# Optimization experiments

Hardware: AMD Instinct MI355X
Metric: run time of the kernel (lower is better)

## Reference

```python
import jax, jax.numpy as jnp
import numpy as np
from math import sqrt

DIM = 256

def setup_inputs() -> dict:
    key = jax.random.key(0)
    k1, k2, k3, k4 = jax.random.split(key, 4)
    B, T, D, H, R = 2, 4096, DIM, 8, 32
    # xavier-uniform-ish scaled params
    def xavier(k, shape, fan_in, fan_out):
        a = sqrt(6.0 / (fan_in + fan_out))
        return jax.random.uniform(k, shape, jnp.float32, -a, a)
    x = jax.random.normal(k1, (B, T, D), jnp.float32)
    Q = xavier(k2, (H, R, D), D, R)
    K = xavier(k3, (H, R, D), D, R)
    VO = xavier(k4, (H, D, D), D, D)
    return {"x": x, "Q": Q, "K": K, "VO": VO}

def reference(x, Q, K, VO):
    # x: [b,t,d]; Q,K: [h,r,d]; VO: [h,d,e]
    d = x.shape[-1]
    q = jnp.einsum('btd,hrd->bhtr', x, Q)          # low-rank query proj
    k = jnp.einsum('bud,hrd->bhur', x, K)          # low-rank key proj
    scores = jnp.einsum('bhtr,bhur->bhtu', q, k) / sqrt(d)
    attn = jax.nn.softmax(scores, axis=-1)         # softmax over u (keys)
    ctx = jnp.einsum('bhtu,bud->bhtd', attn, x)    # values are raw x
    out = jnp.einsum('bhtd,hde->bte', ctx, VO)     # fused value-output proj, summed over heads
    return out
```

## Files before the change

### kernel.cpp

```cpp
#include <hip/hip_runtime.h>
#include <hip/hip_bf16.h>
#include <cstdint>
#include <cstddef>

typedef __attribute__((ext_vector_type(8))) __bf16 bf16x8;
typedef __attribute__((ext_vector_type(4))) float f32x4;
typedef __attribute__((ext_vector_type(16))) float f32x16;

#define MFMA16(a, b, c) __builtin_amdgcn_mfma_f32_16x16x32_bf16((a), (b), (c), 0, 0, 0)
#define MFMA32(a, b, c) __builtin_amdgcn_mfma_f32_32x32x16_bf16((a), (b), (c), 0, 0, 0)
#define MFMA8(a, b, c)  __builtin_amdgcn_mfma_f32_32x32x16_fp8_fp8((a), (b), (c), 0, 0, 0)

__device__ __forceinline__ f32x16 zf16() {
    f32x16 z;
    #pragma unroll
    for (int r = 0; r < 16; ++r) z[r] = 0.f;
    return z;
}

__device__ __forceinline__ void swap32(unsigned& a, unsigned& b) {
    asm("v_permlane32_swap_b32 %0, %1" : "+v"(a), "+v"(b));
}

__global__ __launch_bounds__(256) void prep(const float* __restrict__ x,
                                            const float* __restrict__ Qw,
                                            const float* __restrict__ Kw,
                                            const float* __restrict__ VO,
                                            unsigned char* __restrict__ x8T,
                                            __bf16* __restrict__ xrow,
                                            __bf16* __restrict__ wb,
                                            __bf16* __restrict__ vot) {
    __shared__ float tile[64][65];
    const int bid = blockIdx.x;
    if (bid < 512) {
        const int b = bid >> 8;
        const int rem = bid & 255;
        const int tt = rem >> 2, dd = rem & 3;
        const int t0 = tt * 64, d0 = dd * 64;
        #pragma unroll
        for (int j = 0; j < 16; ++j) {
            int idx = j * 256 + threadIdx.x;
            int t = idx >> 6, d = idx & 63;
            float v = x[((size_t)(b * 4096 + t0 + t)) * 256 + d0 + d];
            tile[t][d] = v;
            xrow[((size_t)(b * 4096 + t0 + t)) * 256 + d0 + d] = (__bf16)v;
        }
        __syncthreads();
        #pragma unroll
        for (int j = 0; j < 8; ++j) {
            int idx = j * 256 + threadIdx.x;
            int d = idx >> 5, tp = idx & 31;
            float v0 = tile[tp * 2][d];
            float v1 = tile[tp * 2 + 1][d];
            int wpk = __builtin_amdgcn_cvt_pk_fp8_f32(v0, v1, 0, false);
            *(unsigned short*)(x8T + (size_t)(b * 256 + d0 + d) * 4096 + t0 + tp * 2) =
                (unsigned short)wpk;
        }
    } else if (bid < 640) {
        const int k = bid - 512;
        const int h = k >> 4;
        const int rem = k & 15;
        const int dt = rem >> 2, et = rem & 3;
        const int d0 = dt * 64, e0 = et * 64;
        #pragma unroll
        for (int j = 0; j < 16; ++j) {
            int idx = j * 256 + threadIdx.x;
            int d = idx >> 6, e = idx & 63;
            tile[d][e] = VO[((size_t)(h * 256 + d0 + d)) * 256 + e0 + e];
        }
        __syncthreads();
        #pragma unroll
        for (int j = 0; j < 16; ++j) {
            int idx = j * 256 + threadIdx.x;
            int e = idx >> 6, d = idx & 63;
            vot[((size_t)(e0 + e)) * 2048 + h * 256 + d0 + d] = (__bf16)tile[d][e];
        }
    } else {
        const float cl = 1.4426950408889634f / 16.0f;
        #pragma unroll
        for (int e = 0; e < 2; ++e) {
            int i = (bid - 640) * 512 + e * 256 + threadIdx.x;
            float v = (i < 65536) ? Qw[i] * cl : Kw[i - 65536];
            wb[i] = (__bf16)v;
        }
    }
}

__global__ __launch_bounds__(256) void proj_kernel(const __bf16* __restrict__ xrow,
                                                   const __bf16* __restrict__ wb,
                                                   __bf16* __restrict__ qo,
                                                   __bf16* __restrict__ ko) {
    const int w = threadIdx.x >> 6;
    const int l = threadIdx.x & 63;
    const int g = l >> 4, c = l & 15;
    const int tg = blockIdx.x * 64 + w * 16;

    bf16x8 af[8];
    #pragma unroll
    for (int kk = 0; kk < 8; ++kk)
        af[kk] = *(const bf16x8*)(xrow + (size_t)(tg + c) * 256 + kk * 32 + g * 8);

    const int b = tg >> 12, t = tg & 4095;
    #pragma unroll
    for (int hs = 0; hs < 16; ++hs) {
        const int h = hs >> 1, s = hs & 1;
        const __bf16* W = wb + (size_t)(s * 8 + h) * 8192;
        f32x4 acc0 = {0.f, 0.f, 0.f, 0.f}, acc1 = {0.f, 0.f, 0.f, 0.f};
        #pragma unroll
        for (int kk = 0; kk < 8; ++kk) {
            bf16x8 b0 = *(const bf16x8*)(W + (size_t)c * 256 + kk * 32 + g * 8);
            bf16x8 b1 = *(const bf16x8*)(W + (size_t)(16 + c) * 256 + kk * 32 + g * 8);
            acc0 = MFMA16(af[kk], b0, acc0);
            acc1 = MFMA16(af[kk], b1, acc1);
        }
        __bf16* outp = s ? ko : qo;
        const size_t obase = (size_t)(b * 8 + h) * 4096 + t;
        #pragma unroll
        for (int i = 0; i < 4; ++i) {
            outp[(obase + 4 * g + i) * 32 + c]      = (__bf16)acc0[i];
            outp[(obase + 4 * g + i) * 32 + 16 + c] = (__bf16)acc1[i];
        }
    }
}


#define MK8FRAG(dst, V, base)                                                  \
    {                                                                          \
        unsigned d0 = 0, d1 = 0;                                               \
        d0 = __builtin_amdgcn_cvt_pk_fp8_f32(V[(base) + 0], V[(base) + 1], d0, false); \
        d0 = __builtin_amdgcn_cvt_pk_fp8_f32(V[(base) + 2], V[(base) + 3], d0, true);  \
        d1 = __builtin_amdgcn_cvt_pk_fp8_f32(V[(base) + 4], V[(base) + 5], d1, false); \
        d1 = __builtin_amdgcn_cvt_pk_fp8_f32(V[(base) + 6], V[(base) + 7], d1, true);  \
        swap32(d0, d1);                                                        \
        union { unsigned u[2]; long l; } z;                                    \
        z.u[0] = d0; z.u[1] = d1;                                              \
        dst = z.l;                                                             \
    }

__global__ __launch_bounds__(512, 2) void attn_kernel(const __bf16* __restrict__ qg,
                                                      const __bf16* __restrict__ kg,
                                                      const unsigned char* __restrict__ x8g,
                                                      __bf16* __restrict__ ctx) {
    __shared__ __align__(16) unsigned char lds[2 * 18432 + 1024];
    unsigned char* xbuf0 = lds;
    unsigned char* xbuf1 = lds + 18432;
    float* scale_base = (float*)(lds + 36864);

    const int bid = blockIdx.x;
    const int bh = bid >> 4;
    const int tt = bid & 15;
    const int b = bh >> 3, h = bh & 7;
    const int t0 = tt * 256;
    const int tid = threadIdx.x;
    const int w = tid >> 6;
    const int l = tid & 63;
    const int l31 = l & 31, hi = l >> 5;

    float* scale_w = scale_base + w * 32;

    const unsigned char* x8b = x8g + (size_t)b * 256 * 4096;
    const __bf16* kg_bh = kg + (size_t)bh * 4096 * 32;

    const int srow = tid >> 1;
    const int soff = (tid & 1) * 32;

    const size_t qoff = ((size_t)bh * 4096 + t0 + w * 32 + l31) * 32;
    const bf16x8 qf0 = *(const bf16x8*)(qg + qoff + hi * 8);
    const bf16x8 qf1 = *(const bf16x8*)(qg + qoff + 16 + hi * 8);

    f32x16 acc[8];
    #pragma unroll
    for (int n = 0; n < 8; ++n)
        #pragma unroll
        for (int r = 0; r < 16; ++r) acc[n][r] = 0.f;

    float lsum = 0.f;

    bf16x8 kA[2][2];
    #pragma unroll
    for (int s = 0; s < 2; ++s)
        #pragma unroll
        for (int st = 0; st < 2; ++st)
            kA[s][st] = *(const bf16x8*)(kg_bh + (size_t)(s * 32 + l31) * 32 + st * 16 + hi * 8);

    {
        const unsigned char* sp = x8b + (size_t)srow * 4096 + soff;
        uint4 la = *(const uint4*)sp;
        uint4 lb = *(const uint4*)(sp + 16);
        unsigned char* dp = xbuf0 + srow * 72 + soff;
        union { uint4 v; unsigned long long q[2]; } ua, ub;
        ua.v = la; ub.v = lb;
        ((unsigned long long*)dp)[0] = ua.q[0];
        ((unsigned long long*)dp)[1] = ua.q[1];
        ((unsigned long long*)(dp + 16))[0] = ub.q[0];
        ((unsigned long long*)(dp + 16))[1] = ub.q[1];
    }
    __syncthreads();

    for (int ut = 0; ut < 64; ++ut) {
        unsigned char* xcur = (ut & 1) ? xbuf1 : xbuf0;
        unsigned char* xnxt = (ut & 1) ? xbuf0 : xbuf1;

        const int u_next = ((ut + 1) & 63) * 64;
        const unsigned char* sp = x8b + (size_t)srow * 4096 + u_next + soff;
        const uint4 la = *(const uint4*)sp;
        const uint4 lb = *(const uint4*)(sp + 16);

        f32x16 s0 = MFMA32(kA[0][0], qf0, zf16());
        s0 = MFMA32(kA[0][1], qf1, s0);
        f32x16 s1 = MFMA32(kA[1][0], qf0, zf16());
        s1 = MFMA32(kA[1][1], qf1, s1);

        if (ut < 63) {
            const __bf16* kp = kg_bh + (size_t)(ut + 1) * 64 * 32;
            #pragma unroll
            for (int s = 0; s < 2; ++s)
                #pragma unroll
                for (int st = 0; st < 2; ++st)
                    kA[s][st] = *(const bf16x8*)(kp + (size_t)(s * 32 + l31) * 32 + st * 16 + hi * 8);
        }

        float rs = 0.f;
        #pragma unroll
        for (int r = 0; r < 16; ++r) {
            float p = __builtin_amdgcn_exp2f(s0[r]);
            s0[r] = p; rs += p;
        }
        #pragma unroll
        for (int r = 0; r < 16; ++r) {
            float p = __builtin_amdgcn_exp2f(s1[r]);
            s1[r] = p; rs += p;
        }
        lsum += rs;

        long pf0, pf1, pf2, pf3;
        MK8FRAG(pf0, s0, 0);
        MK8FRAG(pf1, s0, 8);
        MK8FRAG(pf2, s1, 0);
        MK8FRAG(pf3, s1, 8);

        __builtin_amdgcn_s_setprio(1);
        #pragma unroll
        for (int kk = 0; kk < 4; ++kk) {
            const long pa = (kk == 0) ? pf0 : (kk == 1) ? pf1 : (kk == 2) ? pf2 : pf3;
            #pragma unroll
            for (int n = 0; n < 8; ++n) {
                const long xb = *(const long*)(xcur + (n * 32 + l31) * 72 + kk * 16 + hi * 8);
                acc[n] = MFMA8(pa, xb, acc[n]);
            }
        }
        __builtin_amdgcn_s_setprio(0);

        {
            unsigned char* dp = xnxt + srow * 72 + soff;
            union { uint4 v; unsigned long long q[2]; } ua, ub;
            ua.v = la; ub.v = lb;
            ((unsigned long long*)dp)[0] = ua.q[0];
            ((unsigned long long*)dp)[1] = ua.q[1];
            ((unsigned long long*)(dp + 16))[0] = ub.q[0];
            ((unsigned long long*)(dp + 16))[1] = ub.q[1];
        }
        __syncthreads();
    }

    lsum += __shfl_xor(lsum, 32);
    const float linv = 1.0f / lsum;
    if (!hi) scale_w[l31] = linv;
    f32x4 iv[4];
    #pragma unroll
    for (int q4 = 0; q4 < 4; ++q4)
        iv[q4] = *(const f32x4*)&scale_w[q4 * 8 + hi * 4];
    #pragma unroll
    for (int n = 0; n < 8; ++n) {
        #pragma unroll
        for (int r = 0; r < 16; ++r) {
            int t = t0 + w * 32 + (r & 3) + 8 * (r >> 2) + 4 * hi;
            int d = n * 32 + l31;
            ctx[((size_t)(b * 4096 + t) * 8 + h) * 256 + d] =
                (__bf16)(acc[n][r] * iv[r >> 2][r & 3]);
        }
    }
}

__global__ __launch_bounds__(256) void gemm_out(const __bf16* __restrict__ ctx,
                                                const __bf16* __restrict__ vot,
                                                float* __restrict__ out) {
    const int bid = blockIdx.x;
    const int mt2 = bid >> 1;
    const int eh = bid & 1;
    const int w = threadIdx.x >> 6;
    const int l = threadIdx.x & 63;
    const int l31 = l & 31, hi = l >> 5;
    const size_t a0row = (size_t)(mt2 * 64 + l31) * 2048;
    const size_t a1row = (size_t)(mt2 * 64 + 32 + l31) * 2048;
    const size_t brow  = (size_t)(eh * 128 + w * 32 + l31) * 2048;
    f32x16 acc0 = zf16(), acc1 = zf16();
    #pragma unroll 4
    for (int kk = 0; kk < 128; ++kk) {
        bf16x8 bfr = *(const bf16x8*)(vot + brow + kk * 16 + hi * 8);
        bf16x8 a0  = *(const bf16x8*)(ctx + a0row + kk * 16 + hi * 8);
        bf16x8 a1  = *(const bf16x8*)(ctx + a1row + kk * 16 + hi * 8);
        acc0 = MFMA32(a0, bfr, acc0);
        acc1 = MFMA32(a1, bfr, acc1);
    }
    const int e = eh * 128 + w * 32 + l31;
    #pragma unroll
    for (int r = 0; r < 16; ++r) {
        int crow = (r & 3) + 8 * (r >> 2) + 4 * hi;
        out[(size_t)(mt2 * 64 + crow) * 256 + e]      = acc0[r];
        out[(size_t)(mt2 * 64 + 32 + crow) * 256 + e] = acc1[r];
    }
}

extern "C" void kernel_launch(void* const* d_in, const int* in_sizes, int n_in,
                              void* d_out, int out_size, void* d_ws, size_t ws_size,
                              hipStream_t stream) {
    const float* x  = (const float*)d_in[0];
    const float* Qw = (const float*)d_in[1];
    const float* Kw = (const float*)d_in[2];
    const float* VO = (const float*)d_in[3];
    float* out = (float*)d_out;

    char* ws = (char*)d_ws;
    unsigned char* x8 = (unsigned char*)(ws);
    __bf16* xrow = (__bf16*)(ws + ((size_t)4 << 20));
    __bf16* qb   = (__bf16*)(ws + ((size_t)8 << 20));
    __bf16* kb   = (__bf16*)(ws + ((size_t)12 << 20));
    __bf16* wb   = (__bf16*)(ws + ((size_t)16 << 20));
    __bf16* vot  = (__bf16*)(ws + ((size_t)17 << 20));
    __bf16* ctx  = (__bf16*)(ws + ((size_t)18 << 20));

    prep<<<896, 256, 0, stream>>>(x, Qw, Kw, VO, x8, xrow, wb, vot);
    proj_kernel<<<128, 256, 0, stream>>>(xrow, wb, qb, kb);
    attn_kernel<<<256, 512, 0, stream>>>(qb, kb, x8, ctx);
    gemm_out<<<256, 256, 0, stream>>>(ctx, vot, out);
}
```

Before: 213.5 us.

## Split attention blocks into 128-query tiles with 256 threads each

Halves the attention block from 512 to 256 threads (4 waves covering 128 queries) and doubles the grid to 512 blocks. Each thread now stages a full 64-byte row of the fp8 x tile into LDS instead of half a row. This gives more blocks across the CUs and better load balance, but each block reloads the whole K and x streams, doubling global and L2 traffic for x8 and K.

```diff
diff --git a/kernel.cpp b/kernel.cpp
--- a/kernel.cpp
+++ b/kernel.cpp
@@ -137,20 +137,20 @@
         dst = z.l;                                                             \
     }
 
-__global__ __launch_bounds__(512, 2) void attn_kernel(const __bf16* __restrict__ qg,
+__global__ __launch_bounds__(256, 2) void attn_kernel(const __bf16* __restrict__ qg,
                                                       const __bf16* __restrict__ kg,
                                                       const unsigned char* __restrict__ x8g,
                                                       __bf16* __restrict__ ctx) {
-    __shared__ __align__(16) unsigned char lds[2 * 18432 + 1024];
+    __shared__ __align__(16) unsigned char lds[2 * 18432 + 512];
     unsigned char* xbuf0 = lds;
     unsigned char* xbuf1 = lds + 18432;
     float* scale_base = (float*)(lds + 36864);
 
     const int bid = blockIdx.x;
-    const int bh = bid >> 4;
-    const int tt = bid & 15;
+    const int bh = bid >> 5;
+    const int tt = bid & 31;
     const int b = bh >> 3, h = bh & 7;
-    const int t0 = tt * 256;
+    const int t0 = tt * 128;
     const int tid = threadIdx.x;
     const int w = tid >> 6;
     const int l = tid & 63;
@@ -161,8 +161,7 @@
     const unsigned char* x8b = x8g + (size_t)b * 256 * 4096;
     const __bf16* kg_bh = kg + (size_t)bh * 4096 * 32;
 
-    const int srow = tid >> 1;
-    const int soff = (tid & 1) * 32;
+    const int srow = tid;
 
     const size_t qoff = ((size_t)bh * 4096 + t0 + w * 32 + l31) * 32;
     const bf16x8 qf0 = *(const bf16x8*)(qg + qoff + hi * 8);
@@ -184,16 +183,22 @@
             kA[s][st] = *(const bf16x8*)(kg_bh + (size_t)(s * 32 + l31) * 32 + st * 16 + hi * 8);
 
     {
-        const unsigned char* sp = x8b + (size_t)srow * 4096 + soff;
+        const unsigned char* sp = x8b + (size_t)srow * 4096;
         uint4 la = *(const uint4*)sp;
         uint4 lb = *(const uint4*)(sp + 16);
-        unsigned char* dp = xbuf0 + srow * 72 + soff;
-        union { uint4 v; unsigned long long q[2]; } ua, ub;
-        ua.v = la; ub.v = lb;
+        uint4 lc = *(const uint4*)(sp + 32);
+        uint4 ld = *(const uint4*)(sp + 48);
+        unsigned char* dp = xbuf0 + srow * 72;
+        union { uint4 v; unsigned long long q[2]; } ua, ub, uc, ud;
+        ua.v = la; ub.v = lb; uc.v = lc; ud.v = ld;
         ((unsigned long long*)dp)[0] = ua.q[0];
         ((unsigned long long*)dp)[1] = ua.q[1];
         ((unsigned long long*)(dp + 16))[0] = ub.q[0];
         ((unsigned long long*)(dp + 16))[1] = ub.q[1];
+        ((unsigned long long*)(dp + 32))[0] = uc.q[0];
+        ((unsigned long long*)(dp + 32))[1] = uc.q[1];
+        ((unsigned long long*)(dp + 48))[0] = ud.q[0];
+        ((unsigned long long*)(dp + 48))[1] = ud.q[1];
     }
     __syncthreads();
 
@@ -202,9 +207,11 @@
         unsigned char* xnxt = (ut & 1) ? xbuf0 : xbuf1;
 
         const int u_next = ((ut + 1) & 63) * 64;
-        const unsigned char* sp = x8b + (size_t)srow * 4096 + u_next + soff;
+        const unsigned char* sp = x8b + (size_t)srow * 4096 + u_next;
         const uint4 la = *(const uint4*)sp;
         const uint4 lb = *(const uint4*)(sp + 16);
+        const uint4 lc = *(const uint4*)(sp + 32);
+        const uint4 ld = *(const uint4*)(sp + 48);
 
         f32x16 s0 = MFMA32(kA[0][0], qf0, zf16());
         s0 = MFMA32(kA[0][1], qf1, s0);
@@ -252,13 +259,17 @@
         __builtin_amdgcn_s_setprio(0);
 
         {
-            unsigned char* dp = xnxt + srow * 72 + soff;
-            union { uint4 v; unsigned long long q[2]; } ua, ub;
-            ua.v = la; ub.v = lb;
+            unsigned char* dp = xnxt + srow * 72;
+            union { uint4 v; unsigned long long q[2]; } ua, ub, uc, ud;
+            ua.v = la; ub.v = lb; uc.v = lc; ud.v = ld;
             ((unsigned long long*)dp)[0] = ua.q[0];
             ((unsigned long long*)dp)[1] = ua.q[1];
             ((unsigned long long*)(dp + 16))[0] = ub.q[0];
             ((unsigned long long*)(dp + 16))[1] = ub.q[1];
+            ((unsigned long long*)(dp + 32))[0] = uc.q[0];
+            ((unsigned long long*)(dp + 32))[1] = uc.q[1];
+            ((unsigned long long*)(dp + 48))[0] = ud.q[0];
+            ((unsigned long long*)(dp + 48))[1] = ud.q[1];
         }
         __syncthreads();
     }
@@ -332,6 +343,6 @@
 
     prep<<<896, 256, 0, stream>>>(x, Qw, Kw, VO, x8, xrow, wb, vot);
     proj_kernel<<<128, 256, 0, stream>>>(xrow, wb, qb, kb);
-    attn_kernel<<<256, 512, 0, stream>>>(qb, kb, x8, ctx);
+    attn_kernel<<<512, 256, 0, stream>>>(qb, kb, x8, ctx);
     gemm_out<<<256, 256, 0, stream>>>(ctx, vot, out);
 }
```

Result: slower. 236.4 us (+10.7%).
